# Kernel optimization log

Hardware: AMD Instinct MI355X
Metric: run time of the kernel (lower is better)

## Reference

```python
import jax, jax.numpy as jnp
import numpy as np

B, N, DIM = 2, 2048, 1024
HEADS, DIM_HEAD = 16, 64
INNER = HEADS * DIM_HEAD  # 1024
SCALE = DIM_HEAD ** -0.5


def setup_inputs() -> dict:
    key = jax.random.key(0)
    ks = jax.random.split(key, 6)
    s = lambda k, shape, fan: jax.random.normal(k, shape, jnp.float32) * (fan ** -0.5)
    return {
        "x": jax.random.normal(ks[0], (B, N, DIM), jnp.float32),
        "similarity": jax.random.normal(ks[1], (B, N), jnp.float32),
        "Wq": s(ks[2], (DIM, INNER), DIM),
        "Wkv": s(ks[3], (DIM, 2 * INNER), DIM),
        "Wo": s(ks[4], (INNER, DIM), INNER),
        "bo": jnp.zeros((DIM,), jnp.float32),
    }


def reference(x, similarity, Wq, Wkv, Wo, bo):
    b, n, _ = x.shape
    h, d = HEADS, DIM_HEAD
    # projections (context = x, self-attention)
    q = (x @ Wq).reshape(b, n, h, d).transpose(0, 2, 1, 3)        # b h n d
    kv = x @ Wkv                                                   # b n 2*inner
    k, v = jnp.split(kv, 2, axis=-1)
    k = k.reshape(b, n, h, d).transpose(0, 2, 1, 3)
    v = v.reshape(b, n, h, d).transpose(0, 2, 1, 3)
    dots = jnp.einsum('bhid,bhjd->bhij', q, k) * SCALE             # b h n n
    # similarity [b,n] -> broadcast as per-query row bias [b,1,n,1]
    dots = dots + similarity[:, None, :, None]
    attn = jax.nn.softmax(dots, axis=-1)
    out = jnp.einsum('bhij,bhjd->bhid', attn, v)                   # b h n d
    out = out.transpose(0, 2, 1, 3).reshape(b, n, h * d)           # b n inner
    return out @ Wo + bo
```

## Files before the change

### kernel.cpp

```cpp
#include <hip/hip_runtime.h>


typedef __attribute__((ext_vector_type(8))) short short8;
typedef __attribute__((ext_vector_type(4))) float float4_;
typedef __attribute__((ext_vector_type(16))) float floatx16;
typedef __attribute__((ext_vector_type(4))) unsigned short ushort4_;
typedef __attribute__((ext_vector_type(4))) unsigned int uint4_;

#define MFMA(a, b, c) __builtin_amdgcn_mfma_f32_16x16x32_bf16((a), (b), (c), 0, 0, 0)
#define MFMA32(a, b, c) __builtin_amdgcn_mfma_f32_32x32x16_bf16((a), (b), (c), 0, 0, 0)

static __device__ __forceinline__ unsigned short f2bf(float f) {
    union { float f; unsigned int u; } v; v.f = f;
    unsigned int r = v.u + 0x7FFFu + ((v.u >> 16) & 1u);
    return (unsigned short)(r >> 16);
}

static __device__ __forceinline__ void gld16(const void* g, void* l) {
    __builtin_amdgcn_global_load_lds(
        (__attribute__((address_space(1))) void*)(g),
        (__attribute__((address_space(3))) void*)(l), 16, 0, 0);
}

__global__ __launch_bounds__(256) void prep(
    const float* __restrict__ X, const float* __restrict__ Wq,
    const float* __restrict__ Wkv, const float* __restrict__ Wo,
    unsigned short* __restrict__ xb, unsigned short* __restrict__ Wt,
    unsigned short* __restrict__ Wot)
{
    const int bid = blockIdx.x, t = threadIdx.x;
    if (bid >= 1024) {
        const int b = bid - 1024;
        const float4_* src = (const float4_*)X;
        ushort4_* dst = (ushort4_*)xb;
        #pragma unroll
        for (int g = 0; g < 8; ++g) {
            const int idx = b * 2048 + g * 256 + t;
            float4_ v = src[idx];
            ushort4_ o;
            o[0] = f2bf(v[0]); o[1] = f2bf(v[1]);
            o[2] = f2bf(v[2]); o[3] = f2bf(v[3]);
            dst[idx] = o;
        }
        return;
    }
    __shared__ float tile[64][65];
    const float* src; unsigned short* dst; int N, kt, nt, drow0;
    if (bid < 256)      { src = Wq;  N = 1024; kt = bid & 15;       nt = bid >> 4;       dst = Wt;  drow0 = nt * 64; }
    else if (bid < 768) { src = Wkv; N = 2048; kt = (bid-256) & 15; nt = (bid-256) >> 4; dst = Wt;  drow0 = 1024 + nt * 64; }
    else                { src = Wo;  N = 1024; kt = (bid-768) & 15; nt = (bid-768) >> 4; dst = Wot; drow0 = nt * 64; }
    const int k0 = kt * 64, n0 = nt * 64;
    const int r0 = t >> 6, c = t & 63;
    #pragma unroll
    for (int i = 0; i < 16; ++i) {
        const int r = i * 4 + r0;
        tile[r][c] = src[(size_t)(k0 + r) * N + n0 + c];
    }
    __syncthreads();
    #pragma unroll
    for (int i = 0; i < 16; ++i) {
        const int rn = i * 4 + r0;
        dst[(size_t)(drow0 + rn) * 1024 + k0 + c] = f2bf(tile[c][rn]);
    }
}

__global__ __launch_bounds__(256) void qkv_gemm2(
    const unsigned short* __restrict__ xb, const unsigned short* __restrict__ Wt,
    unsigned short* __restrict__ q_ws, unsigned short* __restrict__ k_ws,
    unsigned short* __restrict__ vt_ws)
{
    __shared__ unsigned short As[128 * 64];
    __shared__ unsigned short Bs[128 * 64];
    const int t = threadIdx.x, wave = t >> 6, lane = t & 63;
    const int L = lane & 15, quad = lane >> 4;
    const int xcd = blockIdx.x & 7, idx = blockIdx.x >> 3;
    const int mb = (xcd >> 1) * 8 + (idx & 7);
    const int nb = (xcd & 1) * 12 + (idx >> 3);
    const int m0 = mb * 128, n0 = nb * 128;
    const int wr = wave >> 1, wc = wave & 1;

    float4_ z = {0.f, 0.f, 0.f, 0.f};
    float4_ acc[4][4];
    #pragma unroll
    for (int i = 0; i < 4; ++i)
        #pragma unroll
        for (int j = 0; j < 4; ++j) acc[i][j] = z;

    const unsigned short* gA[4]; const unsigned short* gB[4];
    unsigned short* lA[4]; unsigned short* lB[4];
    #pragma unroll
    for (int j = 0; j < 4; ++j) {
        const int cid = wave * 256 + j * 64 + lane;
        const int row = cid >> 3, pc = cid & 7;
        const int lch = pc ^ (row & 7);
        gA[j] = xb + (size_t)(m0 + row) * 1024 + lch * 8;
        gB[j] = Wt + (size_t)(n0 + row) * 1024 + lch * 8;
        lA[j] = As + wave * 2048 + j * 512;
        lB[j] = Bs + wave * 2048 + j * 512;
    }

    for (int kc = 0; kc < 1024; kc += 64) {
        #pragma unroll
        for (int j = 0; j < 4; ++j) {
            gld16(gA[j] + kc, lA[j]);
            gld16(gB[j] + kc, lB[j]);
        }
        __syncthreads();
        #pragma unroll
        for (int ks = 0; ks < 2; ++ks) {
            short8 af[4], bfr[4];
            #pragma unroll
            for (int mt = 0; mt < 4; ++mt) {
                const int rl = wr * 64 + mt * 16 + L;
                af[mt] = *(const short8*)(As + rl * 64 + (((ks * 4 + quad) ^ (L & 7)) << 3));
            }
            #pragma unroll
            for (int nt = 0; nt < 4; ++nt) {
                const int rl = wc * 64 + nt * 16 + L;
                bfr[nt] = *(const short8*)(Bs + rl * 64 + (((ks * 4 + quad) ^ (L & 7)) << 3));
            }
            #pragma unroll
            for (int mt = 0; mt < 4; ++mt)
                #pragma unroll
                for (int nt = 0; nt < 4; ++nt)
                    acc[mt][nt] = MFMA(af[mt], bfr[nt], acc[mt][nt]);
        }
        __syncthreads();
    }

    const int b = m0 >> 11;
    const int type = n0 >> 10;
    #pragma unroll
    for (int mt = 0; mt < 4; ++mt) {
        const int m = (m0 & 2047) + wr * 64 + mt * 16 + quad * 4;
        #pragma unroll
        for (int nt = 0; nt < 4; ++nt) {
            const int cl = (n0 & 1023) + wc * 64 + nt * 16 + L;
            const int h = cl >> 6, d = cl & 63;
            float4_ v = acc[mt][nt];
            if (type == 0) {
                unsigned short* p = q_ws + ((size_t)(b * 16 + h) * 2048 + m) * 64 + d;
                #pragma unroll
                for (int r = 0; r < 4; ++r) p[(size_t)r * 64] = f2bf(v[r] * 0.18033688011f);
            } else if (type == 1) {
                unsigned short* p = k_ws + ((size_t)(b * 16 + h) * 2048 + m) * 64 + d;
                #pragma unroll
                for (int r = 0; r < 4; ++r) p[(size_t)r * 64] = f2bf(v[r]);
            } else {
                ushort4_ pk;
                pk[0] = f2bf(v[0]); pk[1] = f2bf(v[1]);
                pk[2] = f2bf(v[2]); pk[3] = f2bf(v[3]);
                *(ushort4_*)(vt_ws + ((size_t)(b * 16 + h) * 64 + d) * 2048 + m) = pk;
            }
        }
    }
}

#define WAITV8 asm volatile("s_waitcnt vmcnt(8)" ::: "memory")
#define WAITV0 asm volatile("s_waitcnt vmcnt(0)" ::: "memory")
#define WAITL0 asm volatile("s_waitcnt lgkmcnt(0)" ::: "memory")
#define BAR    __builtin_amdgcn_s_barrier()

__global__ __launch_bounds__(256, 2) void attn_fwd10(
    const unsigned short* __restrict__ q_ws,
    const unsigned short* __restrict__ k_ws,
    const unsigned short* __restrict__ vt_ws,
    unsigned short* __restrict__ o2)
{
    __shared__ unsigned short pool[32768];
    __shared__ float lsd[2][2][2][32];
    const int t = threadIdx.x, wave = t >> 6, lane = t & 63;
    const int l32 = lane & 31, hi = lane >> 5;
    const int qg = wave & 1, kh = wave >> 1;
    const int xcd = blockIdx.x & 7, loc = blockIdx.x >> 3;
    const int bh = xcd * 4 + (loc >> 4);
    const int qb = loc & 15;

    const unsigned short* Kp = k_ws + (size_t)bh * 2048 * 64;
    const unsigned short* Vt = vt_ws + (size_t)bh * 64 * 2048;

    short8 qf[2][4];
    #pragma unroll
    for (int qt = 0; qt < 2; ++qt) {
        const unsigned short* Qp = q_ws
            + ((size_t)(bh * 2048 + qb * 128 + qg * 64 + qt * 32 + l32)) * 64 + hi * 8;
        #pragma unroll
        for (int k = 0; k < 4; ++k) qf[qt][k] = *(const short8*)(Qp + k * 16);
    }
    WAITV0;

    const unsigned short* kg[4]; const unsigned short* vg[4];
    unsigned short* kdst[4]; unsigned short* vdst[4];
    #pragma unroll
    for (int g = 0; g < 4; ++g) {
        const int cid = g * 128 + qg * 64 + lane;
        const int kr = cid >> 3;
        const int kl = (cid & 7) ^ (kr & 7);
        const int pr = (kr & ~12) | ((kr & 4) << 1) | ((kr & 8) >> 1);
        kg[g] = Kp + (size_t)(kh * 1024 + pr) * 64 + kl * 8;
        vg[g] = Vt + (size_t)kr * 2048 + kh * 1024 + kl * 8;
        kdst[g] = pool + kh * 8192 + g * 1024 + qg * 512;
        vdst[g] = pool + 16384 + kh * 8192 + g * 1024 + qg * 512;
    }

#define STAGE10(p_, it_) do {                                                 \
    const int ko_ = (it_) * 4096;                                             \
    const int vo_ = (it_) * 64;                                               \
    _Pragma("unroll")                                                         \
    for (int g = 0; g < 4; ++g) gld16(kg[g] + ko_, kdst[g] + (p_) * 4096);    \
    _Pragma("unroll")                                                         \
    for (int g = 0; g < 4; ++g) gld16(vg[g] + vo_, vdst[g] + (p_) * 4096);    \
} while (0)

    floatx16 o00, o01, o10, o11;
    #pragma unroll
    for (int r = 0; r < 16; ++r) { o00[r] = 0.f; o01[r] = 0.f; o10[r] = 0.f; o11[r] = 0.f; }
    float lsum0 = 0.f, lsum1 = 0.f;

    STAGE10(0, 0);
    const int sw = l32 & 7;

    #pragma unroll 1
    for (int it = 0; it < 16; ++it) {
        const int p = it & 1;
        if (it + 1 < 16) { STAGE10(p ^ 1, it + 1); WAITV8; }
        else             { WAITV0; }
        BAR;

        const unsigned short* kb = pool + kh * 8192 + p * 4096;
        const unsigned short* vb = pool + 16384 + kh * 8192 + p * 4096;

        floatx16 s00, s01, s10, s11;
        #pragma unroll
        for (int r = 0; r < 16; ++r) { s00[r] = 0.f; s01[r] = 0.f; s10[r] = 0.f; s11[r] = 0.f; }
        #pragma unroll
        for (int k = 0; k < 4; ++k) {
            const int off = (((2 * k + hi) ^ sw) << 3);
            short8 k0 = *(const short8*)(kb + l32 * 64 + off);
            short8 k1 = *(const short8*)(kb + (32 + l32) * 64 + off);
            s00 = MFMA32(k0, qf[0][k], s00); s01 = MFMA32(k1, qf[0][k], s01);
            s10 = MFMA32(k0, qf[1][k], s10); s11 = MFMA32(k1, qf[1][k], s11);
        }

        unsigned int pkA0[8], pkA1[8], pkB0[8], pkB1[8];
        #pragma unroll
        for (int d = 0; d < 8; ++d) {
            union { float f; unsigned int u; } a0, b0, a1, b1;
            a0.f = __builtin_amdgcn_exp2f(s00[2 * d]);
            b0.f = __builtin_amdgcn_exp2f(s00[2 * d + 1]);
            a1.f = __builtin_amdgcn_exp2f(s01[2 * d]);
            b1.f = __builtin_amdgcn_exp2f(s01[2 * d + 1]);
            lsum0 += (a0.f + b0.f) + (a1.f + b1.f);
            pkA0[d] = __builtin_amdgcn_perm(b0.u, a0.u, 0x07060302u);
            pkA1[d] = __builtin_amdgcn_perm(b1.u, a1.u, 0x07060302u);
        }
        #pragma unroll
        for (int d = 0; d < 8; ++d) {
            union { float f; unsigned int u; } a0, b0, a1, b1;
            a0.f = __builtin_amdgcn_exp2f(s10[2 * d]);
            b0.f = __builtin_amdgcn_exp2f(s10[2 * d + 1]);
            a1.f = __builtin_amdgcn_exp2f(s11[2 * d]);
            b1.f = __builtin_amdgcn_exp2f(s11[2 * d + 1]);
            lsum1 += (a0.f + b0.f) + (a1.f + b1.f);
            pkB0[d] = __builtin_amdgcn_perm(b0.u, a0.u, 0x07060302u);
            pkB1[d] = __builtin_amdgcn_perm(b1.u, a1.u, 0x07060302u);
        }

        #pragma unroll
        for (int w = 0; w < 4; ++w) {
            const int c = 2 * w + hi;
            const int voff = ((c ^ sw) << 3);
            short8 vf0 = *(const short8*)(vb + l32 * 64 + voff);
            short8 vf1 = *(const short8*)(vb + (32 + l32) * 64 + voff);
            uint4_ pwA, pwB;
            if (w == 0)      { pwA[0]=pkA0[0]; pwA[1]=pkA0[1]; pwA[2]=pkA0[2]; pwA[3]=pkA0[3];
                               pwB[0]=pkB0[0]; pwB[1]=pkB0[1]; pwB[2]=pkB0[2]; pwB[3]=pkB0[3]; }
            else if (w == 1) { pwA[0]=pkA0[4]; pwA[1]=pkA0[5]; pwA[2]=pkA0[6]; pwA[3]=pkA0[7];
                               pwB[0]=pkB0[4]; pwB[1]=pkB0[5]; pwB[2]=pkB0[6]; pwB[3]=pkB0[7]; }
            else if (w == 2) { pwA[0]=pkA1[0]; pwA[1]=pkA1[1]; pwA[2]=pkA1[2]; pwA[3]=pkA1[3];
                               pwB[0]=pkB1[0]; pwB[1]=pkB1[1]; pwB[2]=pkB1[2]; pwB[3]=pkB1[3]; }
            else             { pwA[0]=pkA1[4]; pwA[1]=pkA1[5]; pwA[2]=pkA1[6]; pwA[3]=pkA1[7];
                               pwB[0]=pkB1[4]; pwB[1]=pkB1[5]; pwB[2]=pkB1[6]; pwB[3]=pkB1[7]; }
            short8 paA = *(short8*)&pwA;
            short8 paB = *(short8*)&pwB;
            o00 = MFMA32(paA, vf0, o00); o01 = MFMA32(paA, vf1, o01);
            o10 = MFMA32(paB, vf0, o10); o11 = MFMA32(paB, vf1, o11);
        }
        WAITL0;
        BAR;
    }

    const float lt0 = lsum0 + __shfl_xor(lsum0, 32);
    const float lt1 = lsum1 + __shfl_xor(lsum1, 32);
    lsd[kh][qg][0][l32] = lt0;
    lsd[kh][qg][1][l32] = lt1;

    float* cb = (float*)pool;
    if (kh == 1) {
        float* base = cb + qg * 4096;
        #pragma unroll
        for (int r = 0; r < 16; ++r) {
            base[(0 * 16 + r) * 64 + lane] = o00[r];
            base[(1 * 16 + r) * 64 + lane] = o01[r];
            base[(2 * 16 + r) * 64 + lane] = o10[r];
            base[(3 * 16 + r) * 64 + lane] = o11[r];
        }
    }
    __syncthreads();
    if (kh == 0) {
        const int b = bh >> 4, h = bh & 15;
        const float* base = cb + qg * 4096;
        unsigned short* obase = o2
            + ((size_t)(b * 2048 + qb * 128 + qg * 64)) * 1024 + h * 64;
        #pragma unroll
        for (int r = 0; r < 16; ++r) {
            const int rowloc = (r & 3) + 8 * (r >> 2) + 4 * hi;
            const float i0 = 1.0f / (lsd[0][qg][0][rowloc] + lsd[1][qg][0][rowloc]);
            const float i1 = 1.0f / (lsd[0][qg][1][rowloc] + lsd[1][qg][1][rowloc]);
            const float a0 = o00[r] + base[(0 * 16 + r) * 64 + lane];
            const float a1 = o01[r] + base[(1 * 16 + r) * 64 + lane];
            const float b0 = o10[r] + base[(2 * 16 + r) * 64 + lane];
            const float b1 = o11[r] + base[(3 * 16 + r) * 64 + lane];
            obase[(size_t)rowloc * 1024 + l32]             = f2bf(a0 * i0);
            obase[(size_t)rowloc * 1024 + 32 + l32]        = f2bf(a1 * i0);
            obase[(size_t)(32 + rowloc) * 1024 + l32]      = f2bf(b0 * i1);
            obase[(size_t)(32 + rowloc) * 1024 + 32 + l32] = f2bf(b1 * i1);
        }
    }
#undef STAGE10
}

__global__ __launch_bounds__(256) void out_gemm2(
    const unsigned short* __restrict__ o2, const unsigned short* __restrict__ Wot,
    const float* __restrict__ bo, float* __restrict__ Out)
{
    __shared__ unsigned short As[128 * 64];
    __shared__ unsigned short Bs[64 * 64];
    const int t = threadIdx.x, wave = t >> 6, lane = t & 63;
    const int L = lane & 15, quad = lane >> 4;
    const int xcd = blockIdx.x & 7, idx = blockIdx.x >> 3;
    const int mb = (xcd >> 1) * 8 + (idx & 7);
    const int nb = (xcd & 1) * 8 + (idx >> 3);
    const int m0 = mb * 128, n0 = nb * 64;
    const int wr = wave >> 1, wc = wave & 1;

    float4_ z = {0.f, 0.f, 0.f, 0.f};
    float4_ acc[4][2];
    #pragma unroll
    for (int i = 0; i < 4; ++i)
        #pragma unroll
        for (int j = 0; j < 2; ++j) acc[i][j] = z;

    const unsigned short* gA[4]; unsigned short* lA[4];
    #pragma unroll
    for (int j = 0; j < 4; ++j) {
        const int cid = wave * 256 + j * 64 + lane;
        const int row = cid >> 3, pc = cid & 7;
        gA[j] = o2 + (size_t)(m0 + row) * 1024 + (pc ^ (row & 7)) * 8;
        lA[j] = As + wave * 2048 + j * 512;
    }
    const unsigned short* gB[2]; unsigned short* lB[2];
    #pragma unroll
    for (int j = 0; j < 2; ++j) {
        const int cid = wave * 128 + j * 64 + lane;
        const int row = cid >> 3, pc = cid & 7;
        gB[j] = Wot + (size_t)(n0 + row) * 1024 + (pc ^ (row & 7)) * 8;
        lB[j] = Bs + wave * 1024 + j * 512;
    }

    for (int kc = 0; kc < 1024; kc += 64) {
        #pragma unroll
        for (int j = 0; j < 4; ++j) gld16(gA[j] + kc, lA[j]);
        #pragma unroll
        for (int j = 0; j < 2; ++j) gld16(gB[j] + kc, lB[j]);
        __syncthreads();
        #pragma unroll
        for (int ks = 0; ks < 2; ++ks) {
            short8 af[4], bfr[2];
            #pragma unroll
            for (int mt = 0; mt < 4; ++mt) {
                const int rl = wr * 64 + mt * 16 + L;
                af[mt] = *(const short8*)(As + rl * 64 + (((ks * 4 + quad) ^ (L & 7)) << 3));
            }
            #pragma unroll
            for (int nt = 0; nt < 2; ++nt) {
                const int rl = wc * 32 + nt * 16 + L;
                bfr[nt] = *(const short8*)(Bs + rl * 64 + (((ks * 4 + quad) ^ (L & 7)) << 3));
            }
            #pragma unroll
            for (int mt = 0; mt < 4; ++mt)
                #pragma unroll
                for (int nt = 0; nt < 2; ++nt)
                    acc[mt][nt] = MFMA(af[mt], bfr[nt], acc[mt][nt]);
        }
        __syncthreads();
    }

    #pragma unroll
    for (int mt = 0; mt < 4; ++mt) {
        const int m = m0 + wr * 64 + mt * 16 + quad * 4;
        #pragma unroll
        for (int nt = 0; nt < 2; ++nt) {
            const int c = n0 + wc * 32 + nt * 16 + L;
            const float bias = bo[c];
            #pragma unroll
            for (int r = 0; r < 4; ++r)
                Out[(size_t)(m + r) * 1024 + c] = acc[mt][nt][r] + bias;
        }
    }
}

extern "C" void kernel_launch(void* const* d_in, const int* in_sizes, int n_in,
                              void* d_out, int out_size, void* d_ws, size_t ws_size,
                              hipStream_t stream) {
    const float* x   = (const float*)d_in[0];
    const float* Wq  = (const float*)d_in[2];
    const float* Wkv = (const float*)d_in[3];
    const float* Wo  = (const float*)d_in[4];
    const float* bo  = (const float*)d_in[5];
    float* out = (float*)d_out;

    char* ws = (char*)d_ws;
    const size_t MB = 1024 * 1024;
    unsigned short* xb   = (unsigned short*)(ws);
    unsigned short* o2   = xb;
    unsigned short* Wt   = (unsigned short*)(ws + 8 * MB);
    unsigned short* Wot  = (unsigned short*)(ws + 14 * MB);
    unsigned short* q_ws = (unsigned short*)(ws + 16 * MB);
    unsigned short* k_ws = (unsigned short*)(ws + 24 * MB);
    unsigned short* vt_ws= (unsigned short*)(ws + 32 * MB);

    prep<<<dim3(1536), dim3(256), 0, stream>>>(x, Wq, Wkv, Wo, xb, Wt, Wot);
    qkv_gemm2<<<dim3(768), dim3(256), 0, stream>>>(xb, Wt, q_ws, k_ws, vt_ws);
    attn_fwd10<<<dim3(512), dim3(256), 0, stream>>>(q_ws, k_ws, vt_ws, o2);
    out_gemm2<<<dim3(512), dim3(256), 0, stream>>>(o2, Wot, bo, out);
}
```

Baseline: 184.4 us.

## Halve attention KV tile to 32 keys per wave for higher occupancy

Shrinks the per-iteration K/V tile in the attention kernel from 64 to 32 keys per key-half, halving LDS use and per-iteration score registers. Launch bounds move from 2 to 4 blocks per CU to exploit the smaller footprint. The V-tile layout and its swizzle change to match the narrower tile. The price is twice as many loop iterations, and with them twice as many barriers and waitcnt syncs, with less work per sync to hide load latency.

```diff
diff --git a/kernel.cpp b/kernel.cpp
--- a/kernel.cpp
+++ b/kernel.cpp
@@ -156,18 +156,18 @@
     }
 }
 
-#define WAITV8 asm volatile("s_waitcnt vmcnt(8)" ::: "memory")
+#define WAITV4 asm volatile("s_waitcnt vmcnt(4)" ::: "memory")
 #define WAITV0 asm volatile("s_waitcnt vmcnt(0)" ::: "memory")
 #define WAITL0 asm volatile("s_waitcnt lgkmcnt(0)" ::: "memory")
 #define BAR    __builtin_amdgcn_s_barrier()
 
-__global__ __launch_bounds__(256, 2) void attn_fwd10(
+__global__ __launch_bounds__(256, 4) void attn_fwd11(
     const unsigned short* __restrict__ q_ws,
     const unsigned short* __restrict__ k_ws,
     const unsigned short* __restrict__ vt_ws,
     unsigned short* __restrict__ o2)
 {
-    __shared__ unsigned short pool[32768];
+    __shared__ unsigned short pool[16384];
     __shared__ float lsd[2][2][2][32];
     const int t = threadIdx.x, wave = t >> 6, lane = t & 63;
     const int l32 = lane & 31, hi = lane >> 5;
@@ -189,27 +189,30 @@
     }
     WAITV0;
 
-    const unsigned short* kg[4]; const unsigned short* vg[4];
-    unsigned short* kdst[4]; unsigned short* vdst[4];
-    #pragma unroll
-    for (int g = 0; g < 4; ++g) {
+    const unsigned short* kg[2]; const unsigned short* vg[2];
+    unsigned short* kdst[2]; unsigned short* vdst[2];
+    #pragma unroll
+    for (int g = 0; g < 2; ++g) {
         const int cid = g * 128 + qg * 64 + lane;
         const int kr = cid >> 3;
         const int kl = (cid & 7) ^ (kr & 7);
         const int pr = (kr & ~12) | ((kr & 4) << 1) | ((kr & 8) >> 1);
         kg[g] = Kp + (size_t)(kh * 1024 + pr) * 64 + kl * 8;
-        vg[g] = Vt + (size_t)kr * 2048 + kh * 1024 + kl * 8;
-        kdst[g] = pool + kh * 8192 + g * 1024 + qg * 512;
-        vdst[g] = pool + 16384 + kh * 8192 + g * 1024 + qg * 512;
-    }
-
-#define STAGE10(p_, it_) do {                                                 \
-    const int ko_ = (it_) * 4096;                                             \
-    const int vo_ = (it_) * 64;                                               \
+        const int vr = cid >> 3, vp = cid & 7;
+        const int vd = vr + 32 * (vp >> 2);
+        const int vkc = (vp & 3) ^ (vr & 3);
+        vg[g] = Vt + (size_t)vd * 2048 + kh * 1024 + vkc * 8;
+        kdst[g] = pool + kh * 4096 + g * 1024 + qg * 512;
+        vdst[g] = pool + 8192 + kh * 4096 + g * 1024 + qg * 512;
+    }
+
+#define STAGE11(p_, it_) do {                                                 \
+    const int ko_ = (it_) * 2048;                     \
+    const int vo_ = (it_) * 32;                     \
     _Pragma("unroll")                                                         \
-    for (int g = 0; g < 4; ++g) gld16(kg[g] + ko_, kdst[g] + (p_) * 4096);    \
+    for (int g = 0; g < 2; ++g) gld16(kg[g] + ko_, kdst[g] + (p_) * 2048);    \
     _Pragma("unroll")                                                         \
-    for (int g = 0; g < 4; ++g) gld16(vg[g] + vo_, vdst[g] + (p_) * 4096);    \
+    for (int g = 0; g < 2; ++g) gld16(vg[g] + vo_, vdst[g] + (p_) * 2048);    \
 } while (0)
 
     floatx16 o00, o01, o10, o11;
@@ -217,70 +220,56 @@
     for (int r = 0; r < 16; ++r) { o00[r] = 0.f; o01[r] = 0.f; o10[r] = 0.f; o11[r] = 0.f; }
     float lsum0 = 0.f, lsum1 = 0.f;
 
-    STAGE10(0, 0);
+    STAGE11(0, 0);
     const int sw = l32 & 7;
+    const int sw2 = l32 & 3;
 
     #pragma unroll 1
-    for (int it = 0; it < 16; ++it) {
+    for (int it = 0; it < 32; ++it) {
         const int p = it & 1;
-        if (it + 1 < 16) { STAGE10(p ^ 1, it + 1); WAITV8; }
+        if (it + 1 < 32) { STAGE11(p ^ 1, it + 1); WAITV4; }
         else             { WAITV0; }
         BAR;
 
-        const unsigned short* kb = pool + kh * 8192 + p * 4096;
-        const unsigned short* vb = pool + 16384 + kh * 8192 + p * 4096;
-
-        floatx16 s00, s01, s10, s11;
-        #pragma unroll
-        for (int r = 0; r < 16; ++r) { s00[r] = 0.f; s01[r] = 0.f; s10[r] = 0.f; s11[r] = 0.f; }
+        const unsigned short* kb = pool + kh * 4096 + p * 2048;
+        const unsigned short* vb = pool + 8192 + kh * 4096 + p * 2048;
+
+        floatx16 s00, s10;
+        #pragma unroll
+        for (int r = 0; r < 16; ++r) { s00[r] = 0.f; s10[r] = 0.f; }
         #pragma unroll
         for (int k = 0; k < 4; ++k) {
             const int off = (((2 * k + hi) ^ sw) << 3);
             short8 k0 = *(const short8*)(kb + l32 * 64 + off);
-            short8 k1 = *(const short8*)(kb + (32 + l32) * 64 + off);
-            s00 = MFMA32(k0, qf[0][k], s00); s01 = MFMA32(k1, qf[0][k], s01);
-            s10 = MFMA32(k0, qf[1][k], s10); s11 = MFMA32(k1, qf[1][k], s11);
-        }
-
-        unsigned int pkA0[8], pkA1[8], pkB0[8], pkB1[8];
+            s00 = MFMA32(k0, qf[0][k], s00);
+            s10 = MFMA32(k0, qf[1][k], s10);
+        }
+
+        unsigned int pkA[8], pkB[8];
         #pragma unroll
         for (int d = 0; d < 8; ++d) {
             union { float f; unsigned int u; } a0, b0, a1, b1;
             a0.f = __builtin_amdgcn_exp2f(s00[2 * d]);
             b0.f = __builtin_amdgcn_exp2f(s00[2 * d + 1]);
-            a1.f = __builtin_amdgcn_exp2f(s01[2 * d]);
-            b1.f = __builtin_amdgcn_exp2f(s01[2 * d + 1]);
-            lsum0 += (a0.f + b0.f) + (a1.f + b1.f);
-            pkA0[d] = __builtin_amdgcn_perm(b0.u, a0.u, 0x07060302u);
-            pkA1[d] = __builtin_amdgcn_perm(b1.u, a1.u, 0x07060302u);
-        }
-        #pragma unroll
-        for (int d = 0; d < 8; ++d) {
-            union { float f; unsigned int u; } a0, b0, a1, b1;
-            a0.f = __builtin_amdgcn_exp2f(s10[2 * d]);
-            b0.f = __builtin_amdgcn_exp2f(s10[2 * d + 1]);
-            a1.f = __builtin_amdgcn_exp2f(s11[2 * d]);
-            b1.f = __builtin_amdgcn_exp2f(s11[2 * d + 1]);
-            lsum1 += (a0.f + b0.f) + (a1.f + b1.f);
-            pkB0[d] = __builtin_amdgcn_perm(b0.u, a0.u, 0x07060302u);
-            pkB1[d] = __builtin_amdgcn_perm(b1.u, a1.u, 0x07060302u);
-        }
-
-        #pragma unroll
-        for (int w = 0; w < 4; ++w) {
+            a1.f = __builtin_amdgcn_exp2f(s10[2 * d]);
+            b1.f = __builtin_amdgcn_exp2f(s10[2 * d + 1]);
+            lsum0 += a0.f + b0.f;
+            lsum1 += a1.f + b1.f;
+            pkA[d] = __builtin_amdgcn_perm(b0.u, a0.u, 0x07060302u);
+            pkB[d] = __builtin_amdgcn_perm(b1.u, a1.u, 0x07060302u);
+        }
+
+        #pragma unroll
+        for (int w = 0; w < 2; ++w) {
             const int c = 2 * w + hi;
-            const int voff = ((c ^ sw) << 3);
+            const int voff = ((c ^ sw2) << 3);
             short8 vf0 = *(const short8*)(vb + l32 * 64 + voff);
-            short8 vf1 = *(const short8*)(vb + (32 + l32) * 64 + voff);
+            short8 vf1 = *(const short8*)(vb + l32 * 64 + 32 + voff);
             uint4_ pwA, pwB;
-            if (w == 0)      { pwA[0]=pkA0[0]; pwA[1]=pkA0[1]; pwA[2]=pkA0[2]; pwA[3]=pkA0[3];
-                               pwB[0]=pkB0[0]; pwB[1]=pkB0[1]; pwB[2]=pkB0[2]; pwB[3]=pkB0[3]; }
-            else if (w == 1) { pwA[0]=pkA0[4]; pwA[1]=pkA0[5]; pwA[2]=pkA0[6]; pwA[3]=pkA0[7];
-                               pwB[0]=pkB0[4]; pwB[1]=pkB0[5]; pwB[2]=pkB0[6]; pwB[3]=pkB0[7]; }
-            else if (w == 2) { pwA[0]=pkA1[0]; pwA[1]=pkA1[1]; pwA[2]=pkA1[2]; pwA[3]=pkA1[3];
-                               pwB[0]=pkB1[0]; pwB[1]=pkB1[1]; pwB[2]=pkB1[2]; pwB[3]=pkB1[3]; }
-            else             { pwA[0]=pkA1[4]; pwA[1]=pkA1[5]; pwA[2]=pkA1[6]; pwA[3]=pkA1[7];
-                               pwB[0]=pkB1[4]; pwB[1]=pkB1[5]; pwB[2]=pkB1[6]; pwB[3]=pkB1[7]; }
+            if (w == 0) { pwA[0]=pkA[0]; pwA[1]=pkA[1]; pwA[2]=pkA[2]; pwA[3]=pkA[3];
+                          pwB[0]=pkB[0]; pwB[1]=pkB[1]; pwB[2]=pkB[2]; pwB[3]=pkB[3]; }
+            else        { pwA[0]=pkA[4]; pwA[1]=pkA[5]; pwA[2]=pkA[6]; pwA[3]=pkA[7];
+                          pwB[0]=pkB[4]; pwB[1]=pkB[5]; pwB[2]=pkB[6]; pwB[3]=pkB[7]; }
             short8 paA = *(short8*)&pwA;
             short8 paB = *(short8*)&pwB;
             o00 = MFMA32(paA, vf0, o00); o01 = MFMA32(paA, vf1, o01);
@@ -327,7 +316,7 @@
             obase[(size_t)(32 + rowloc) * 1024 + 32 + l32] = f2bf(b1 * i1);
         }
     }
-#undef STAGE10
+#undef STAGE11
 }
 
 __global__ __launch_bounds__(256) void out_gemm2(
@@ -432,6 +421,6 @@
 
     prep<<<dim3(1536), dim3(256), 0, stream>>>(x, Wq, Wkv, Wo, xb, Wt, Wot);
     qkv_gemm2<<<dim3(768), dim3(256), 0, stream>>>(xb, Wt, q_ws, k_ws, vt_ws);
-    attn_fwd10<<<dim3(512), dim3(256), 0, stream>>>(q_ws, k_ws, vt_ws, o2);
+    attn_fwd11<<<dim3(512), dim3(256), 0, stream>>>(q_ws, k_ws, vt_ws, o2);
     out_gemm2<<<dim3(512), dim3(256), 0, stream>>>(o2, Wot, bo, out);
 }
```

New measurement: 399.6 us. 2.17x slower.
